# Performance work log

Measured on AMD Instinct MI355X. Metric: run time of the kernel, lower is better.

## Reference

```python
import jax, jax.numpy as jnp
import numpy as np

D_MODEL, D_K, D_V, H = 512, 64, 64, 8
B, NQ, NK = 2, 4096, 4096


def setup_inputs() -> dict:
    key = jax.random.key(0)
    ks = jax.random.split(key, 11)
    def xavier(k, shape):
        fan_in, fan_out = shape[1], shape[0]
        lim = jnp.sqrt(6.0 / (fan_in + fan_out))
        return jax.random.uniform(k, shape, jnp.float32, -lim, lim)
    return {
        "queries": jax.random.normal(ks[0], (B, NQ, D_MODEL), jnp.float32),
        "keys": jax.random.normal(ks[1], (B, NK, D_MODEL), jnp.float32),
        "values": jax.random.normal(ks[2], (B, NK, D_MODEL), jnp.float32),
        "Wq": xavier(ks[3], (H * D_K, D_MODEL)),
        "bq": jnp.zeros((H * D_K,), jnp.float32),
        "Wk": xavier(ks[4], (H * D_K, D_MODEL)),
        "bk": jnp.zeros((H * D_K,), jnp.float32),
        "Wv": xavier(ks[5], (H * D_V, D_MODEL)),
        "bv": jnp.zeros((H * D_V,), jnp.float32),
        "Wo": xavier(ks[6], (D_MODEL, H * D_V)),
        "bo": jnp.zeros((D_MODEL,), jnp.float32),
    }


def reference(queries, keys, values, Wq, bq, Wk, bk, Wv, bv, Wo, bo):
    b_s, nq, _ = queries.shape
    nk = keys.shape[1]
    # QKV projections (torch Linear: x @ W.T + b)
    q = (queries @ Wq.T + bq).reshape(b_s, nq, H, D_K).transpose(0, 2, 1, 3)  # b h nq dk
    k = (keys @ Wk.T + bk).reshape(b_s, nk, H, D_K).transpose(0, 2, 1, 3)     # b h nk dk
    v = (values @ Wv.T + bv).reshape(b_s, nk, H, D_V).transpose(0, 2, 1, 3)   # b h nk dv
    att = jnp.einsum("bhqd,bhkd->bhqk", q, k) / jnp.sqrt(jnp.float32(D_K))
    att = jax.nn.softmax(att, axis=-1)
    # dropout is identity in eval mode
    out = jnp.einsum("bhqk,bhkd->bhqd", att, v)
    out = out.transpose(0, 2, 1, 3).reshape(b_s, nq, H * D_V)
    return out @ Wo.T + bo
```

## Files before the change

kernel.cpp:

```cpp
#include <hip/hip_runtime.h>
#include <hip/hip_bf16.h>


typedef __attribute__((ext_vector_type(8))) short bf16x8;
typedef __attribute__((ext_vector_type(4))) float f32x4;

#define SEQ  4096
#define DM   512
#define FPAD 72
#define VPAD 136
#define QSCALE 0.18033688011112042f
#define FSHIFT 16.0f

__device__ inline float fast_exp2(float x) {
#if __has_builtin(__builtin_amdgcn_exp2f)
    return __builtin_amdgcn_exp2f(x);
#else
    return __expf(x * 0.69314718056f);
#endif
}

__device__ inline unsigned pk2(float x, float y) {
#if __has_builtin(__builtin_amdgcn_cvt_pk_bf16_f32)
    typedef __attribute__((ext_vector_type(2))) __bf16 bf16x2_t;
    bf16x2_t h = __builtin_amdgcn_cvt_pk_bf16_f32(x, y);
    return *(unsigned*)&h;
#else
    unsigned ux = __float_as_uint(x);
    unsigned uy = __float_as_uint(y);
    ux += 0x7fff + ((ux >> 16) & 1);
    uy += 0x7fff + ((uy >> 16) & 1);
    return (ux >> 16) | (uy & 0xffff0000u);
#endif
}

__global__ __launch_bounds__(256) void cvt_w(
    const float* __restrict__ w0, const float* __restrict__ w1,
    const float* __restrict__ w2, const float* __restrict__ w3,
    __hip_bfloat16* __restrict__ o0, __hip_bfloat16* __restrict__ o1,
    __hip_bfloat16* __restrict__ o2, __hip_bfloat16* __restrict__ o3)
{
    const float* w = (blockIdx.y == 0) ? w0 : (blockIdx.y == 1) ? w1
                   : (blockIdx.y == 2) ? w2 : w3;
    __hip_bfloat16* o = (blockIdx.y == 0) ? o0 : (blockIdx.y == 1) ? o1
                      : (blockIdx.y == 2) ? o2 : o3;
    const int i = (blockIdx.x * 256 + threadIdx.x) * 4;
    float4 v = *(const float4*)&w[i];
    uint2 p;
    p.x = pk2(v.x, v.y);
    p.y = pk2(v.z, v.w);
    *(uint2*)&((unsigned short*)o)[i] = p;
}

__global__ __launch_bounds__(256) void qkv_proj(
    const float* __restrict__ Xq, const float* __restrict__ Xk, const float* __restrict__ Xv,
    const __hip_bfloat16* __restrict__ Wq16, const __hip_bfloat16* __restrict__ Wk16,
    const __hip_bfloat16* __restrict__ Wv16,
    const float* __restrict__ bq, const float* __restrict__ bk, const float* __restrict__ bv,
    __hip_bfloat16* __restrict__ Oq, __hip_bfloat16* __restrict__ Ok,
    __hip_bfloat16* __restrict__ Ovt)
{
    const int z = blockIdx.z;
    const float* A          = (z == 0) ? Xq : (z == 1) ? Xk : Xv;
    const __hip_bfloat16* W = (z == 0) ? Wq16 : (z == 1) ? Wk16 : Wv16;
    const float* bias       = (z == 0) ? bq : (z == 1) ? bk : bv;

    __shared__ __align__(16) short As[64 * 32];
    __shared__ __align__(16) short Ws2[128 * 32];

    const int bm   = blockIdx.x * 64;
    const int bn   = blockIdx.y * 128;
    const int tid  = threadIdx.x;
    const int wave = tid >> 6;
    const int lane = tid & 63;
    const int quad = lane >> 4;
    const int l16  = lane & 15;

    const int srow = tid >> 2;
    const int scol = (tid & 3) * 8;

    f32x4 acc[8] = {};

    float4 a0 = *(const float4*)&A[(size_t)(bm + srow) * DM + scol];
    float4 a1 = *(const float4*)&A[(size_t)(bm + srow) * DM + scol + 4];
    bf16x8 w0 = *(const bf16x8*)&W[(size_t)(bn + srow) * DM + scol];
    bf16x8 w1 = *(const bf16x8*)&W[(size_t)(bn + srow + 64) * DM + scol];

    for (int k0 = 0; k0 < DM; k0 += 32) {
        uint4 pa = {pk2(a0.x, a0.y), pk2(a0.z, a0.w), pk2(a1.x, a1.y), pk2(a1.z, a1.w)};

        __syncthreads();
        *(uint4*)&As[srow * 32 + scol] = pa;
        *(bf16x8*)&Ws2[srow * 32 + scol] = w0;
        *(bf16x8*)&Ws2[(srow + 64) * 32 + scol] = w1;
        __syncthreads();

        if (k0 + 32 < DM) {
            a0 = *(const float4*)&A[(size_t)(bm + srow) * DM + k0 + 32 + scol];
            a1 = *(const float4*)&A[(size_t)(bm + srow) * DM + k0 + 32 + scol + 4];
            w0 = *(const bf16x8*)&W[(size_t)(bn + srow) * DM + k0 + 32 + scol];
            w1 = *(const bf16x8*)&W[(size_t)(bn + srow + 64) * DM + k0 + 32 + scol];
        }

        bf16x8 a = *(bf16x8*)&As[(wave * 16 + l16) * 32 + quad * 8];
#pragma unroll
        for (int nt = 0; nt < 8; nt++) {
            bf16x8 b = *(bf16x8*)&Ws2[(nt * 16 + l16) * 32 + quad * 8];
            acc[nt] = __builtin_amdgcn_mfma_f32_16x16x32_bf16(a, b, acc[nt], 0, 0, 0);
        }
    }

    if (z == 2) {
        const int row0 = bm + wave * 16 + quad * 4;
        const int b    = row0 >> 12;
        const int seq0 = row0 & 4095;
        unsigned short* Vt = (unsigned short*)Ovt;
#pragma unroll
        for (int nt = 0; nt < 8; nt++) {
            const int col = bn + nt * 16 + l16;
            const float bv_ = bias[col];
            uint2 pk;
            pk.x = pk2(acc[nt][0] + bv_, acc[nt][1] + bv_);
            pk.y = pk2(acc[nt][2] + bv_, acc[nt][3] + bv_);
            *(uint2*)&Vt[((size_t)(b * 512 + col)) * 4096 + seq0] = pk;
        }
    } else {
        unsigned short* C = (unsigned short*)((z == 0) ? Oq : Ok);
        const float scale = (z == 0) ? QSCALE : 1.0f;
        const size_t row0 = bm + wave * 16 + quad * 4;
#pragma unroll
        for (int nt = 0; nt < 8; nt++) {
            const int col = bn + nt * 16 + l16;
            const float bv_ = bias[col];
            unsigned u01 = pk2((acc[nt][0] + bv_) * scale, (acc[nt][1] + bv_) * scale);
            unsigned u23 = pk2((acc[nt][2] + bv_) * scale, (acc[nt][3] + bv_) * scale);
            C[(row0 + 0) * DM + col] = (unsigned short)(u01 & 0xffff);
            C[(row0 + 1) * DM + col] = (unsigned short)(u01 >> 16);
            C[(row0 + 2) * DM + col] = (unsigned short)(u23 & 0xffff);
            C[(row0 + 3) * DM + col] = (unsigned short)(u23 >> 16);
        }
    }
}

__global__ __launch_bounds__(512, 4) void flash_attn(
    const __hip_bfloat16* __restrict__ Q,
    const __hip_bfloat16* __restrict__ K,
    const __hip_bfloat16* __restrict__ Vt,
    __hip_bfloat16* __restrict__ O)
{
    __shared__ __align__(16) short Qs[128 * FPAD];
    __shared__ __align__(16) short Ks[128 * FPAD];
    __shared__ __align__(16) short Vs[64 * VPAD];

    const int q0 = blockIdx.x * 128;
    const int bh = blockIdx.y;

    const int tid  = threadIdx.x;
    const int wave = tid >> 6;
    const int lane = tid & 63;
    const int quad = lane >> 4;
    const int l16  = lane & 15;
    const int qw   = wave * 16;

    const __hip_bfloat16* Qb = Q + (size_t)(bh >> 3) * SEQ * DM + (bh & 7) * 64;
    const __hip_bfloat16* Kb = K + (size_t)(bh >> 3) * SEQ * DM + (bh & 7) * 64;
    const __hip_bfloat16* Vb = Vt + (size_t)bh * 64 * SEQ;
    __hip_bfloat16*       Ob = O + (size_t)(bh >> 3) * SEQ * DM + (bh & 7) * 64;

    const int kr = tid >> 3;
    const int kc = (tid & 7) * 8;
    const int vr = tid >> 4;
    const int vc = (tid & 15) * 8;

#pragma unroll
    for (int i = 0; i < 2; i++)
        *(bf16x8*)&Qs[(kr + i * 64) * FPAD + kc] =
            *(const bf16x8*)&Qb[(size_t)(q0 + kr + i * 64) * DM + kc];

    const __hip_bfloat16* kg = Kb + (size_t)kr * DM + kc;
    const __hip_bfloat16* vg = Vb + (size_t)vr * SEQ + vc;

    bf16x8 kp[2], vp[2];
#pragma unroll
    for (int i = 0; i < 2; i++) {
        kp[i] = *(const bf16x8*)(kg + (size_t)i * 64 * DM);
        vp[i] = *(const bf16x8*)(vg + (size_t)i * 32 * SEQ);
    }

    __syncthreads();

    bf16x8 bq[2];
#pragma unroll
    for (int ks = 0; ks < 2; ks++)
        bq[ks] = *(bf16x8*)&Qs[(qw + l16) * FPAD + ks * 32 + quad * 8];

    bf16x8 ones;
#pragma unroll
    for (int j = 0; j < 8; j++) ones[j] = (short)0x3F80;

    const short* ksb = &Ks[l16 * FPAD + quad * 8];
    const short* vsb = &Vs[l16 * VPAD + quad * 8];
    const short* psb = &Qs[(qw + l16) * FPAD + quad * 8];
    short*       psw = &Qs[(qw + l16) * FPAD + quad * 4];

    f32x4 oacc[4] = {};
    f32x4 lacc = {};

    for (int kv0 = 0; kv0 < SEQ; kv0 += 128) {
        __syncthreads();
#pragma unroll
        for (int i = 0; i < 2; i++) {
            *(bf16x8*)&Ks[(kr + i * 64) * FPAD + kc] = kp[i];
            *(bf16x8*)&Vs[(vr + i * 32) * VPAD + vc] = vp[i];
        }
        __syncthreads();

        kg += (size_t)128 * DM;
        vg += 128;
        if (kv0 + 128 < SEQ) {
#pragma unroll
            for (int i = 0; i < 2; i++) {
                kp[i] = *(const bf16x8*)(kg + (size_t)i * 64 * DM);
                vp[i] = *(const bf16x8*)(vg + (size_t)i * 32 * SEQ);
            }
        }

#pragma unroll
        for (int kh = 0; kh < 2; kh++) {
            f32x4 s[4] = {};
            __builtin_amdgcn_s_setprio(1);
#pragma unroll
            for (int ks = 0; ks < 2; ks++) {
#pragma unroll
                for (int nt = 0; nt < 4; nt++) {
                    bf16x8 ak = *(const bf16x8*)&ksb[(kh * 64 + nt * 16) * FPAD + ks * 32];
                    s[nt] = __builtin_amdgcn_mfma_f32_16x16x32_bf16(
                        ak, bq[ks], s[nt], 0, 0, 0);
                }
            }
            __builtin_amdgcn_s_setprio(0);

#pragma unroll
            for (int nt = 0; nt < 4; nt++) {
                float p0 = fast_exp2(s[nt][0] - FSHIFT);
                float p1 = fast_exp2(s[nt][1] - FSHIFT);
                float p2 = fast_exp2(s[nt][2] - FSHIFT);
                float p3 = fast_exp2(s[nt][3] - FSHIFT);
                uint2 pk;
                pk.x = pk2(p0, p1);
                pk.y = pk2(p2, p3);
                *(uint2*)&psw[nt * 16] = pk;
            }

            __builtin_amdgcn_s_setprio(1);
#pragma unroll
            for (int ks = 0; ks < 2; ks++) {
                bf16x8 av[4];
#pragma unroll
                for (int dt = 0; dt < 4; dt++)
                    av[dt] = *(const bf16x8*)&vsb[dt * 16 * VPAD + kh * 64 + ks * 32];
                bf16x8 bp = *(const bf16x8*)&psb[ks * 32];
#pragma unroll
                for (int dt = 0; dt < 4; dt++)
                    oacc[dt] = __builtin_amdgcn_mfma_f32_16x16x32_bf16(
                        av[dt], bp, oacc[dt], 0, 0, 0);
                lacc = __builtin_amdgcn_mfma_f32_16x16x32_bf16(
                    ones, bp, lacc, 0, 0, 0);
            }
            __builtin_amdgcn_s_setprio(0);
        }
    }

    unsigned short* Op = (unsigned short*)Ob;
    const float inv = 1.0f / lacc[0];
    const int q = q0 + qw + l16;
#pragma unroll
    for (int dt = 0; dt < 4; dt++) {
        uint2 ov;
        ov.x = pk2(oacc[dt][0] * inv, oacc[dt][1] * inv);
        ov.y = pk2(oacc[dt][2] * inv, oacc[dt][3] * inv);
        *(uint2*)&Op[(size_t)q * DM + dt * 16 + quad * 4] = ov;
    }
}

__global__ __launch_bounds__(256) void out_proj(
    const __hip_bfloat16* __restrict__ A,
    const __hip_bfloat16* __restrict__ W,
    const float* __restrict__ bias,
    float* __restrict__ C)
{
    __shared__ __align__(16) short As[64 * 32];
    __shared__ __align__(16) short Ws2[128 * 32];

    const int bm   = blockIdx.x * 64;
    const int bn   = blockIdx.y * 128;
    const int tid  = threadIdx.x;
    const int wave = tid >> 6;
    const int lane = tid & 63;
    const int quad = lane >> 4;
    const int l16  = lane & 15;

    const int srow = tid >> 2;
    const int scol = (tid & 3) * 8;

    f32x4 acc[8] = {};

    bf16x8 ap = *(const bf16x8*)&A[(size_t)(bm + srow) * DM + scol];
    bf16x8 w0 = *(const bf16x8*)&W[(size_t)(bn + srow) * DM + scol];
    bf16x8 w1 = *(const bf16x8*)&W[(size_t)(bn + srow + 64) * DM + scol];

    for (int k0 = 0; k0 < DM; k0 += 32) {
        __syncthreads();
        *(bf16x8*)&As[srow * 32 + scol] = ap;
        *(bf16x8*)&Ws2[srow * 32 + scol] = w0;
        *(bf16x8*)&Ws2[(srow + 64) * 32 + scol] = w1;
        __syncthreads();

        if (k0 + 32 < DM) {
            ap = *(const bf16x8*)&A[(size_t)(bm + srow) * DM + k0 + 32 + scol];
            w0 = *(const bf16x8*)&W[(size_t)(bn + srow) * DM + k0 + 32 + scol];
            w1 = *(const bf16x8*)&W[(size_t)(bn + srow + 64) * DM + k0 + 32 + scol];
        }

        bf16x8 a = *(bf16x8*)&As[(wave * 16 + l16) * 32 + quad * 8];
#pragma unroll
        for (int nt = 0; nt < 8; nt++) {
            bf16x8 b = *(bf16x8*)&Ws2[(nt * 16 + l16) * 32 + quad * 8];
            acc[nt] = __builtin_amdgcn_mfma_f32_16x16x32_bf16(a, b, acc[nt], 0, 0, 0);
        }
    }

#pragma unroll
    for (int nt = 0; nt < 8; nt++) {
        const int col = bn + nt * 16 + l16;
        const float bv_ = bias[col];
#pragma unroll
        for (int r = 0; r < 4; r++) {
            const int row = bm + wave * 16 + quad * 4 + r;
            C[(size_t)row * DM + col] = acc[nt][r] + bv_;
        }
    }
}

extern "C" void kernel_launch(void* const* d_in, const int* in_sizes, int n_in,
                              void* d_out, int out_size, void* d_ws, size_t ws_size,
                              hipStream_t stream) {
    const float* queries = (const float*)d_in[0];
    const float* keys    = (const float*)d_in[1];
    const float* values  = (const float*)d_in[2];
    const float* Wq = (const float*)d_in[3];
    const float* bq = (const float*)d_in[4];
    const float* Wk = (const float*)d_in[5];
    const float* bk = (const float*)d_in[6];
    const float* Wv = (const float*)d_in[7];
    const float* bv = (const float*)d_in[8];
    const float* Wo = (const float*)d_in[9];
    const float* bo = (const float*)d_in[10];
    float* out = (float*)d_out;

    const size_t MS = (size_t)2 * SEQ * DM;
    const size_t WN = (size_t)DM * DM;
    __hip_bfloat16* q_ws  = (__hip_bfloat16*)d_ws;
    __hip_bfloat16* k_ws  = q_ws + MS;
    __hip_bfloat16* vt_ws = k_ws + MS;
    __hip_bfloat16* o_ws  = vt_ws + MS;
    __hip_bfloat16* wq16  = o_ws + MS;
    __hip_bfloat16* wk16  = wq16 + WN;
    __hip_bfloat16* wv16  = wk16 + WN;
    __hip_bfloat16* wo16  = wv16 + WN;

    dim3 blk(256);

    cvt_w<<<dim3(256, 4), blk, 0, stream>>>(Wq, Wk, Wv, Wo, wq16, wk16, wv16, wo16);

    qkv_proj<<<dim3(128, 4, 3), blk, 0, stream>>>(
        queries, keys, values, wq16, wk16, wv16, bq, bk, bv, q_ws, k_ws, vt_ws);

    flash_attn<<<dim3(32, 16), dim3(512), 0, stream>>>(q_ws, k_ws, vt_ws, o_ws);

    out_proj<<<dim3(128, 4), blk, 0, stream>>>(o_ws, wo16, bo, out);
}
```

Baseline: 251.5 us.

## Use 32x32 MFMA in flash attention with register-resident P via permlane swap

Reworks the attention kernel so each of four waves handles 32 query rows with 32x32x16 bf16 MFMAs instead of eight waves using 16x16x32. The probability tile stays in registers: it is packed to bf16 and rearranged across lane halves with permlane32_swap (or a shuffle fallback) rather than round-tripped through LDS. The row sum is accumulated with scalar adds instead of an extra ones-matrix MFMA, and the Q tile is loaded directly from global memory into registers. The gains come from fewer LDS writes and syncs and fewer MFMA instructions. In exchange each thread holds more registers, and with 256 threads per block the per-block occupancy pattern changes.

```diff
diff --git a/kernel.cpp b/kernel.cpp
--- a/kernel.cpp
+++ b/kernel.cpp
@@ -4,6 +4,8 @@
 
 typedef __attribute__((ext_vector_type(8))) short bf16x8;
 typedef __attribute__((ext_vector_type(4))) float f32x4;
+typedef __attribute__((ext_vector_type(16))) float f32x16;
+typedef __attribute__((ext_vector_type(2))) int int2v;
 
 #define SEQ  4096
 #define DM   512
@@ -31,6 +33,20 @@
     ux += 0x7fff + ((ux >> 16) & 1);
     uy += 0x7fff + ((uy >> 16) & 1);
     return (ux >> 16) | (uy & 0xffff0000u);
+#endif
+}
+
+__device__ inline int2v swap_half(unsigned a, unsigned b, int h) {
+#if __has_builtin(__builtin_amdgcn_permlane32_swap)
+    (void)h;
+    return __builtin_amdgcn_permlane32_swap((int)a, (int)b, false, false);
+#else
+    unsigned ax = (unsigned)__shfl_xor((int)a, 32);
+    unsigned bx = (unsigned)__shfl_xor((int)b, 32);
+    int2v r;
+    r.x = h ? (int)bx : (int)a;
+    r.y = h ? (int)b  : (int)ax;
+    return r;
 #endif
 }
 
@@ -142,25 +158,22 @@
     }
 }
 
-__global__ __launch_bounds__(512, 4) void flash_attn(
+__global__ __launch_bounds__(256, 4) void flash_attn(
     const __hip_bfloat16* __restrict__ Q,
     const __hip_bfloat16* __restrict__ K,
     const __hip_bfloat16* __restrict__ Vt,
     __hip_bfloat16* __restrict__ O)
 {
-    __shared__ __align__(16) short Qs[128 * FPAD];
     __shared__ __align__(16) short Ks[128 * FPAD];
     __shared__ __align__(16) short Vs[64 * VPAD];
 
-    const int q0 = blockIdx.x * 128;
-    const int bh = blockIdx.y;
-
-    const int tid  = threadIdx.x;
+    const int q0  = blockIdx.x * 128;
+    const int bh  = blockIdx.y;
+    const int tid = threadIdx.x;
     const int wave = tid >> 6;
     const int lane = tid & 63;
-    const int quad = lane >> 4;
-    const int l16  = lane & 15;
-    const int qw   = wave * 16;
+    const int L = lane & 31;
+    const int h = lane >> 5;
 
     const __hip_bfloat16* Qb = Q + (size_t)(bh >> 3) * SEQ * DM + (bh & 7) * 64;
     const __hip_bfloat16* Kb = K + (size_t)(bh >> 3) * SEQ * DM + (bh & 7) * 64;
@@ -172,46 +185,34 @@
     const int vr = tid >> 4;
     const int vc = (tid & 15) * 8;
 
-#pragma unroll
-    for (int i = 0; i < 2; i++)
-        *(bf16x8*)&Qs[(kr + i * 64) * FPAD + kc] =
-            *(const bf16x8*)&Qb[(size_t)(q0 + kr + i * 64) * DM + kc];
+    const int qrow = q0 + wave * 32 + L;
+    bf16x8 bq[4];
+#pragma unroll
+    for (int db = 0; db < 4; db++)
+        bq[db] = *(const bf16x8*)&Qb[(size_t)qrow * DM + db * 16 + h * 8];
 
     const __hip_bfloat16* kg = Kb + (size_t)kr * DM + kc;
     const __hip_bfloat16* vg = Vb + (size_t)vr * SEQ + vc;
 
-    bf16x8 kp[2], vp[2];
-#pragma unroll
-    for (int i = 0; i < 2; i++) {
-        kp[i] = *(const bf16x8*)(kg + (size_t)i * 64 * DM);
-        vp[i] = *(const bf16x8*)(vg + (size_t)i * 32 * SEQ);
-    }
-
-    __syncthreads();
-
-    bf16x8 bq[2];
-#pragma unroll
-    for (int ks = 0; ks < 2; ks++)
-        bq[ks] = *(bf16x8*)&Qs[(qw + l16) * FPAD + ks * 32 + quad * 8];
-
-    bf16x8 ones;
-#pragma unroll
-    for (int j = 0; j < 8; j++) ones[j] = (short)0x3F80;
-
-    const short* ksb = &Ks[l16 * FPAD + quad * 8];
-    const short* vsb = &Vs[l16 * VPAD + quad * 8];
-    const short* psb = &Qs[(qw + l16) * FPAD + quad * 8];
-    short*       psw = &Qs[(qw + l16) * FPAD + quad * 4];
-
-    f32x4 oacc[4] = {};
-    f32x4 lacc = {};
+    bf16x8 kp[4], vp[4];
+#pragma unroll
+    for (int i = 0; i < 4; i++) {
+        kp[i] = *(const bf16x8*)(kg + (size_t)i * 32 * DM);
+        vp[i] = *(const bf16x8*)(vg + (size_t)i * 16 * SEQ);
+    }
+
+    const short* ksb = &Ks[L * FPAD + h * 8];
+    const short* vsb = &Vs[L * VPAD + h * 8];
+
+    f32x16 oacc[2] = {};
+    float lsum = 0.0f;
 
     for (int kv0 = 0; kv0 < SEQ; kv0 += 128) {
         __syncthreads();
 #pragma unroll
-        for (int i = 0; i < 2; i++) {
-            *(bf16x8*)&Ks[(kr + i * 64) * FPAD + kc] = kp[i];
-            *(bf16x8*)&Vs[(vr + i * 32) * VPAD + vc] = vp[i];
+        for (int i = 0; i < 4; i++) {
+            *(bf16x8*)&Ks[(kr + i * 32) * FPAD + kc] = kp[i];
+            *(bf16x8*)&Vs[(vr + i * 16) * VPAD + vc] = vp[i];
         }
         __syncthreads();
 
@@ -219,68 +220,69 @@
         vg += 128;
         if (kv0 + 128 < SEQ) {
 #pragma unroll
-            for (int i = 0; i < 2; i++) {
-                kp[i] = *(const bf16x8*)(kg + (size_t)i * 64 * DM);
-                vp[i] = *(const bf16x8*)(vg + (size_t)i * 32 * SEQ);
+            for (int i = 0; i < 4; i++) {
+                kp[i] = *(const bf16x8*)(kg + (size_t)i * 32 * DM);
+                vp[i] = *(const bf16x8*)(vg + (size_t)i * 16 * SEQ);
             }
         }
 
 #pragma unroll
-        for (int kh = 0; kh < 2; kh++) {
-            f32x4 s[4] = {};
+        for (int kb = 0; kb < 4; kb++) {
+            f32x16 s = {};
             __builtin_amdgcn_s_setprio(1);
 #pragma unroll
-            for (int ks = 0; ks < 2; ks++) {
-#pragma unroll
-                for (int nt = 0; nt < 4; nt++) {
-                    bf16x8 ak = *(const bf16x8*)&ksb[(kh * 64 + nt * 16) * FPAD + ks * 32];
-                    s[nt] = __builtin_amdgcn_mfma_f32_16x16x32_bf16(
-                        ak, bq[ks], s[nt], 0, 0, 0);
-                }
+            for (int db = 0; db < 4; db++) {
+                bf16x8 ak = *(const bf16x8*)&ksb[(kb * 32) * FPAD + db * 16];
+                s = __builtin_amdgcn_mfma_f32_32x32x16_bf16(ak, bq[db], s, 0, 0, 0);
             }
             __builtin_amdgcn_s_setprio(0);
 
 #pragma unroll
-            for (int nt = 0; nt < 4; nt++) {
-                float p0 = fast_exp2(s[nt][0] - FSHIFT);
-                float p1 = fast_exp2(s[nt][1] - FSHIFT);
-                float p2 = fast_exp2(s[nt][2] - FSHIFT);
-                float p3 = fast_exp2(s[nt][3] - FSHIFT);
-                uint2 pk;
-                pk.x = pk2(p0, p1);
-                pk.y = pk2(p2, p3);
-                *(uint2*)&psw[nt * 16] = pk;
-            }
+            for (int r = 0; r < 16; r++) s[r] = fast_exp2(s[r] - FSHIFT);
+
+            unsigned pk_[8];
+#pragma unroll
+            for (int j = 0; j < 8; j++) pk_[j] = pk2(s[2 * j], s[2 * j + 1]);
+
+#pragma unroll
+            for (int j = 0; j < 8; j++)
+                lsum += __uint_as_float(pk_[j] << 16)
+                      + __uint_as_float(pk_[j] & 0xffff0000u);
+
+            int2v w0 = swap_half(pk_[0], pk_[2], h);
+            int2v w1 = swap_half(pk_[1], pk_[3], h);
+            int2v w2 = swap_half(pk_[4], pk_[6], h);
+            int2v w3 = swap_half(pk_[5], pk_[7], h);
+            uint4 f0u = {(unsigned)w0.x, (unsigned)w1.x, (unsigned)w0.y, (unsigned)w1.y};
+            uint4 f1u = {(unsigned)w2.x, (unsigned)w3.x, (unsigned)w2.y, (unsigned)w3.y};
+            bf16x8 fg0 = *(bf16x8*)&f0u;
+            bf16x8 fg1 = *(bf16x8*)&f1u;
 
             __builtin_amdgcn_s_setprio(1);
 #pragma unroll
-            for (int ks = 0; ks < 2; ks++) {
-                bf16x8 av[4];
-#pragma unroll
-                for (int dt = 0; dt < 4; dt++)
-                    av[dt] = *(const bf16x8*)&vsb[dt * 16 * VPAD + kh * 64 + ks * 32];
-                bf16x8 bp = *(const bf16x8*)&psb[ks * 32];
-#pragma unroll
-                for (int dt = 0; dt < 4; dt++)
-                    oacc[dt] = __builtin_amdgcn_mfma_f32_16x16x32_bf16(
-                        av[dt], bp, oacc[dt], 0, 0, 0);
-                lacc = __builtin_amdgcn_mfma_f32_16x16x32_bf16(
-                    ones, bp, lacc, 0, 0, 0);
+            for (int dvb = 0; dvb < 2; dvb++) {
+                bf16x8 av0 = *(const bf16x8*)&vsb[(dvb * 32) * VPAD + kb * 32];
+                bf16x8 av1 = *(const bf16x8*)&vsb[(dvb * 32) * VPAD + kb * 32 + 16];
+                oacc[dvb] = __builtin_amdgcn_mfma_f32_32x32x16_bf16(av0, fg0, oacc[dvb], 0, 0, 0);
+                oacc[dvb] = __builtin_amdgcn_mfma_f32_32x32x16_bf16(av1, fg1, oacc[dvb], 0, 0, 0);
             }
             __builtin_amdgcn_s_setprio(0);
         }
     }
 
+    const float tot = lsum + __shfl_xor(lsum, 32);
+    const float inv = 1.0f / tot;
+
     unsigned short* Op = (unsigned short*)Ob;
-    const float inv = 1.0f / lacc[0];
-    const int q = q0 + qw + l16;
-#pragma unroll
-    for (int dt = 0; dt < 4; dt++) {
-        uint2 ov;
-        ov.x = pk2(oacc[dt][0] * inv, oacc[dt][1] * inv);
-        ov.y = pk2(oacc[dt][2] * inv, oacc[dt][3] * inv);
-        *(uint2*)&Op[(size_t)q * DM + dt * 16 + quad * 4] = ov;
-    }
+#pragma unroll
+    for (int dvb = 0; dvb < 2; dvb++)
+#pragma unroll
+        for (int b = 0; b < 4; b++) {
+            uint2 ov;
+            ov.x = pk2(oacc[dvb][4 * b + 0] * inv, oacc[dvb][4 * b + 1] * inv);
+            ov.y = pk2(oacc[dvb][4 * b + 2] * inv, oacc[dvb][4 * b + 3] * inv);
+            *(uint2*)&Op[(size_t)qrow * DM + dvb * 32 + b * 8 + h * 4] = ov;
+        }
 }
 
 __global__ __launch_bounds__(256) void out_proj(
@@ -376,7 +378,7 @@
     qkv_proj<<<dim3(128, 4, 3), blk, 0, stream>>>(
         queries, keys, values, wq16, wk16, wv16, bq, bk, bv, q_ws, k_ws, vt_ws);
 
-    flash_attn<<<dim3(32, 16), dim3(512), 0, stream>>>(q_ws, k_ws, vt_ws, o_ws);
+    flash_attn<<<dim3(32, 16), blk, 0, stream>>>(q_ws, k_ws, vt_ws, o_ws);
 
     out_proj<<<dim3(128, 4), blk, 0, stream>>>(o_ws, wo16, bo, out);
 }
```

Result: no change. 251.3 us (-0.1%).
